# Kernel tuning notes

Hardware: AMD Instinct MI355X
Metric: run time of the kernel (lower is better)

The kernel has to match this reference:

```python
import jax, jax.numpy as jnp
import numpy as np

H = 16      # num_heads
HD = 64     # head_dim
W = 1024    # local window size
G = 256     # number of global tokens
EPS = 1e-6
NEG = -1e30


def setup_inputs() -> dict:
    key = jax.random.key(0)
    ks = jax.random.split(key, 7)
    B, S, D = 1, 8192, 1024
    inner = H * HD
    s = 0.02
    return {
        "x": jax.random.normal(ks[0], (B, S, D), jnp.float32),
        "norm_w": jnp.ones((D,), jnp.float32),
        "w_q": jax.random.normal(ks[1], (D, inner), jnp.float32) * s,
        "w_k": jax.random.normal(ks[2], (D, inner), jnp.float32) * s,
        "w_v": jax.random.normal(ks[3], (D, inner), jnp.float32) * s,
        "w_out": jax.random.normal(ks[4], (inner, D), jnp.float32) * s,
        "scorer_w": jax.random.normal(ks[5], (D, 1), jnp.float32) * s,
        "scorer_b": jnp.zeros((1,), jnp.float32),
    }


def reference(x, norm_w, w_q, w_k, w_v, w_out, scorer_w, scorer_b):
    B, S, D = x.shape
    # pre-norm (RMSNorm)
    h = x * jax.lax.rsqrt(jnp.mean(x * x, axis=-1, keepdims=True) + EPS) * norm_w

    def proj(w):  # [B,S,D] -> [B,H,S,HD]
        return jnp.einsum('bsd,de->bse', h, w).reshape(B, S, H, HD).transpose(0, 2, 1, 3)

    q, k, v = proj(w_q), proj(w_k), proj(w_v)
    scale = HD ** -0.5

    # --- local block attention (non-overlapping causal windows) ---
    nW = S // W
    qw = q.reshape(B, H, nW, W, HD)
    kw = k.reshape(B, H, nW, W, HD)
    vw = v.reshape(B, H, nW, W, HD)
    ll = jnp.einsum('bhnqd,bhnkd->bhnqk', qw, kw) * scale  # [B,H,nW,W,W]
    cm = jnp.tril(jnp.ones((W, W), bool))
    ll = jnp.where(cm, ll, NEG).reshape(B, H, S, W)

    # --- sparse global attention over top-G important tokens ---
    scores = (jnp.einsum('bsd,do->bso', h, scorer_w) + scorer_b)[..., 0]  # [B,S]
    _, idx = jax.lax.top_k(scores, G)                                     # [B,G]
    kg = jnp.take_along_axis(k, idx[:, None, :, None], axis=2)            # [B,H,G,HD]
    vg = jnp.take_along_axis(v, idx[:, None, :, None], axis=2)
    lg = jnp.einsum('bhsd,bhgd->bhsg', q, kg) * scale                     # [B,H,S,G]
    pos = jnp.arange(S)
    gmask = idx[:, None, None, :] <= pos[None, None, :, None]             # causal: global pos <= query pos
    lg = jnp.where(gmask, lg, NEG)

    # --- joint softmax over local window + global tokens ---
    attn = jax.nn.softmax(jnp.concatenate([ll, lg], axis=-1), axis=-1)    # [B,H,S,W+G]
    a_loc = attn[..., :W].reshape(B, H, nW, W, W)
    o = jnp.einsum('bhnqk,bhnkd->bhnqd', a_loc, vw).reshape(B, H, S, HD)
    o = o + jnp.einsum('bhsg,bhgd->bhsd', attn[..., W:], vg)

    o = o.transpose(0, 2, 1, 3).reshape(B, S, H * HD)
    return x + jnp.einsum('bse,ed->bsd', o, w_out)  # residual
```

## Files before the change

### kernel.cpp

```cpp
#include <hip/hip_runtime.h>
#include <stdint.h>

#define S_LEN 8192
#define DIM   1024
#define NH    16
#define HD    64
#define WIN   1024
#define GTOK  256
#define QKV_STRIDE (3 * DIM)

typedef __attribute__((ext_vector_type(8))) short bf16x8;
typedef __attribute__((ext_vector_type(4))) float f32x4;
typedef __attribute__((ext_vector_type(16))) float f32x16;
typedef unsigned short u16;

__device__ __forceinline__ u16 f2bf(float f) {
  union { float f; uint32_t u; } v; v.f = f;
  uint32_t r = v.u + 0x7fffu + ((v.u >> 16) & 1u);
  return (u16)(r >> 16);
}
__device__ __forceinline__ float bf2f(u16 b) {
  union { uint32_t u; float f; } v; v.u = ((uint32_t)b) << 16;
  return v.f;
}
__device__ __forceinline__ uint32_t cvtpk(float a, float b) {
  uint32_t r;
  asm("v_cvt_pk_bf16_f32 %0, %1, %2" : "=v"(r) : "v"(a), "v"(b));
  return r;
}

__device__ __forceinline__ void gload_lds16(const void* g, void* l) {
  __builtin_amdgcn_global_load_lds((const __attribute__((address_space(1))) void*)g,
                                   (__attribute__((address_space(3))) void*)l, 16, 0, 0);
}

__global__ __launch_bounds__(256) void rmsnorm_score_kernel(
    const float* __restrict__ x, const float* __restrict__ nw,
    const float* __restrict__ sw, const float* __restrict__ sb,
    u16* __restrict__ h, float* __restrict__ scores) {
  int row = blockIdx.x, tid = threadIdx.x;
  const float4* xr = (const float4*)(x + (size_t)row * DIM);
  float4 v = xr[tid];
  float ss = v.x * v.x + v.y * v.y + v.z * v.z + v.w * v.w;
#pragma unroll
  for (int o = 32; o >= 1; o >>= 1) ss += __shfl_xor(ss, o);
  __shared__ float red[4], red2[4];
  int wv = tid >> 6;
  if ((tid & 63) == 0) red[wv] = ss;
  __syncthreads();
  ss = red[0] + red[1] + red[2] + red[3];
  float rn = rsqrtf(ss * (1.0f / DIM) + 1e-6f);
  float4 w4 = ((const float4*)nw)[tid];
  float h0 = v.x * rn * w4.x, h1 = v.y * rn * w4.y;
  float h2 = v.z * rn * w4.z, h3 = v.w * rn * w4.w;
  uint64_t pack = (uint64_t)f2bf(h0) | ((uint64_t)f2bf(h1) << 16) |
                  ((uint64_t)f2bf(h2) << 32) | ((uint64_t)f2bf(h3) << 48);
  *(uint64_t*)(h + (size_t)row * DIM + tid * 4) = pack;
  float4 s4 = ((const float4*)sw)[tid];
  float sc = h0 * s4.x + h1 * s4.y + h2 * s4.z + h3 * s4.w;
#pragma unroll
  for (int o = 32; o >= 1; o >>= 1) sc += __shfl_xor(sc, o);
  if ((tid & 63) == 0) red2[wv] = sc;
  __syncthreads();
  if (tid == 0) scores[row] = red2[0] + red2[1] + red2[2] + red2[3] + sb[0];
}

__global__ __launch_bounds__(256) void transpose_w_kernel(
    const float* __restrict__ wq, const float* __restrict__ wk,
    const float* __restrict__ wv, const float* __restrict__ wo,
    u16* __restrict__ wqkvT, u16* __restrict__ woutT) {
  __shared__ float tile[32][33];
  int z = blockIdx.z;
  const float* src = (z == 0) ? wq : (z == 1) ? wk : (z == 2) ? wv : wo;
  u16* dst = (z < 3) ? (wqkvT + (size_t)z * DIM * DIM) : woutT;
  int tx = threadIdx.x, ty = threadIdx.y;
  int n0 = blockIdx.x * 32, k0 = blockIdx.y * 32;
#pragma unroll
  for (int i = 0; i < 4; i++)
    tile[ty + i * 8][tx] = src[(size_t)(k0 + ty + i * 8) * DIM + n0 + tx];
  __syncthreads();
#pragma unroll
  for (int i = 0; i < 4; i++)
    dst[(size_t)(n0 + ty + i * 8) * DIM + k0 + tx] = f2bf(tile[tx][ty + i * 8]);
}

__global__ __launch_bounds__(256) void topk_init_kernel(int* __restrict__ cnt) {
  cnt[blockIdx.x * 256 + threadIdx.x] = 0;
}

__global__ __launch_bounds__(256) void topk_count_kernel(
    const float* __restrict__ scores, int* __restrict__ cnt) {
  __shared__ float sj[1024];
  int jbase = blockIdx.y * 1024;
  for (int t = threadIdx.x; t < 1024; t += 256) sj[t] = scores[jbase + t];
  __syncthreads();
  int i = blockIdx.x * 256 + threadIdx.x;
  float my = scores[i];
  int c = 0;
  const float4* s4 = (const float4*)sj;
#pragma unroll 4
  for (int j = 0; j < 256; j++) {
    float4 v = s4[j];
    int b = jbase + j * 4;
    c += (v.x > my) || (v.x == my && (b + 0) < i);
    c += (v.y > my) || (v.y == my && (b + 1) < i);
    c += (v.z > my) || (v.z == my && (b + 2) < i);
    c += (v.w > my) || (v.w == my && (b + 3) < i);
  }
  if (c) atomicAdd(&cnt[i], c);
}

__global__ __launch_bounds__(256) void topk_scatter_kernel(
    const int* __restrict__ cnt, int* __restrict__ gidx) {
  int i = blockIdx.x * 256 + threadIdx.x;
  int c = cnt[i];
  if (c < GTOK) gidx[c] = i;
}

__global__ __launch_bounds__(128) void gather_kernel(
    const u16* __restrict__ qkv, const int* __restrict__ gidx,
    u16* __restrict__ kg, u16* __restrict__ vg) {
  int g = blockIdx.x, t = threadIdx.x;
  size_t src = (size_t)gidx[g] * QKV_STRIDE;
  *(bf16x8*)(kg + (size_t)g * DIM + t * 8) = *(const bf16x8*)(qkv + src + DIM + t * 8);
  *(bf16x8*)(vg + (size_t)g * DIM + t * 8) = *(const bf16x8*)(qkv + src + 2 * DIM + t * 8);
}

template <int RESID>
__global__ __launch_bounds__(256) void gemm_bt_kernel(
    const u16* __restrict__ A, const u16* __restrict__ B,
    u16* __restrict__ Cb, float* __restrict__ Cf, const float* __restrict__ X,
    int M, int N, int K) {
  __shared__ u16 aT[128 * 64];
  __shared__ u16 bT[128 * 64];
  int tid = threadIdx.x;
  int wave = tid >> 6, lane = tid & 63;
  int l15 = lane & 15, l4 = lane >> 4;
  int wr = (wave >> 1) * 64, wc = (wave & 1) * 64;
  int mbase = blockIdx.x * 128, nbase = blockIdx.y * 128;
  f32x4 acc[4][4] = {};
  for (int kt = 0; kt < K; kt += 64) {
#pragma unroll
    for (int c = 0; c < 4; c++) {
      int chunk = wave * 4 + c;
      int row = chunk * 8 + (lane >> 3);
      int col = kt + (lane & 7) * 8;
      gload_lds16(A + (size_t)(mbase + row) * K + col, aT + chunk * 512);
      gload_lds16(B + (size_t)(nbase + row) * K + col, bT + chunk * 512);
    }
    __syncthreads();
#pragma unroll
    for (int kk = 0; kk < 2; kk++) {
      bf16x8 af[4], bfr[4];
#pragma unroll
      for (int i = 0; i < 4; i++) {
        af[i]  = *(const bf16x8*)(aT + (wr + i * 16 + l15) * 64 + kk * 32 + l4 * 8);
        bfr[i] = *(const bf16x8*)(bT + (wc + i * 16 + l15) * 64 + kk * 32 + l4 * 8);
      }
#pragma unroll
      for (int i = 0; i < 4; i++)
#pragma unroll
        for (int j = 0; j < 4; j++)
          acc[i][j] = __builtin_amdgcn_mfma_f32_16x16x32_bf16(af[i], bfr[j], acc[i][j], 0, 0, 0);
    }
    __syncthreads();
  }
#pragma unroll
  for (int i = 0; i < 4; i++) {
#pragma unroll
    for (int j = 0; j < 4; j++) {
#pragma unroll
      for (int r = 0; r < 4; r++) {
        int row = mbase + wr + i * 16 + l4 * 4 + r;
        int col = nbase + wc + j * 16 + l15;
        float v = acc[i][j][r];
        if (RESID) Cf[(size_t)row * N + col] = X[(size_t)row * N + col] + v;
        else       Cb[(size_t)row * N + col] = f2bf(v);
      }
    }
  }
}

__global__ __launch_bounds__(512) void attn_kernel(
    const u16* __restrict__ qkv, const u16* __restrict__ kg,
    const u16* __restrict__ vg, const int* __restrict__ gidx,
    u16* __restrict__ o) {
  __shared__ u16 kT[2][64][72];
  __shared__ u16 vT[2][64][72];
  __shared__ int gposLds[2][64];
  const int tid = threadIdx.x, wave = tid >> 6, lane = tid & 63;
  const int l31 = lane & 31, hi = lane >> 5;
  const int win = blockIdx.x >> 1, pair = blockIdx.x & 1;
  const int wbase = win * WIN;
  const int hoff = blockIdx.y * HD;

  const int skey = tid >> 3, sd8 = (tid & 7) * 8;
  const int vcol = skey ^ ((sd8 >> 4) << 4);

  bf16x8 nk, nv;
  int ng = 0;
  {
    const u16* base = qkv + (size_t)(wbase + skey) * QKV_STRIDE + hoff + sd8;
    nk = *(const bf16x8*)(base + DIM);
    nv = *(const bf16x8*)(base + 2 * DIM);
  }

  for (int sp = 0; sp < 2; sp++) {
    const int j = sp ? (3 - pair) : pair;
    const int qsbase = wbase + j * 256;
    const int nLocal = (j + 1) * 4;
    const int nTiles = nLocal + GTOK / 64;
    const int qrow = qsbase + wave * 32 + l31;
    const int qwmax = qsbase + wave * 32 + 31;

    bf16x8 qf[4];
    {
      const float SC2 = 0.125f * 1.44269504088896f;
      const u16* qptr = qkv + (size_t)qrow * QKV_STRIDE + hoff + hi * 8;
#pragma unroll
      for (int ks = 0; ks < 4; ks++) {
        bf16x8 raw = *(const bf16x8*)(qptr + ks * 16);
        bf16x8 sc;
#pragma unroll
        for (int jj = 0; jj < 8; jj++) sc[jj] = (short)f2bf(bf2f((u16)raw[jj]) * SC2);
        qf[ks] = sc;
      }
    }

    f32x16 acc0 = {}, acc1 = {};
    float mr = -3.0e38f, lr = 0.f;

    __syncthreads();

    for (int t = 0; t < nTiles; t++) {
      const int p = t & 1;
      const bool isLocal = (t < nLocal);
      const int tbase = wbase + t * 64;
      *(bf16x8*)(&kT[p][skey][sd8]) = nk;
#pragma unroll
      for (int jj = 0; jj < 8; jj++) vT[p][sd8 + jj][vcol] = (u16)nv[jj];
      if (!isLocal && tid < 64) gposLds[p][tid] = ng;
      {
        const int nt = t + 1;
        const u16 *ksrc = nullptr, *vsrc = nullptr;
        if (nt < nLocal) {
          const u16* base = qkv + (size_t)(wbase + nt * 64 + skey) * QKV_STRIDE + hoff + sd8;
          ksrc = base + DIM; vsrc = base + 2 * DIM;
        } else if (nt < nTiles) {
          size_t grow = (size_t)((nt - nLocal) * 64 + skey) * DIM + hoff + sd8;
          ksrc = kg + grow; vsrc = vg + grow;
          if (tid < 64) ng = gidx[(nt - nLocal) * 64 + tid];
        } else if (sp == 0) {
          const u16* base = qkv + (size_t)(wbase + skey) * QKV_STRIDE + hoff + sd8;
          ksrc = base + DIM; vsrc = base + 2 * DIM;
        }
        if (ksrc) { nk = *(const bf16x8*)(ksrc); nv = *(const bf16x8*)(vsrc); }
      }
      __syncthreads();

      if (isLocal && tbase > qwmax) continue;

      float sv[32];
      __builtin_amdgcn_s_setprio(1);
#pragma unroll
      for (int kb = 0; kb < 2; kb++) {
        const u16* krow = &kT[p][kb * 32 + l31][hi * 8];
        bf16x8 k0 = *(const bf16x8*)(krow);
        bf16x8 k1 = *(const bf16x8*)(krow + 16);
        bf16x8 k2 = *(const bf16x8*)(krow + 32);
        bf16x8 k3 = *(const bf16x8*)(krow + 48);
        f32x16 z = {};
        z = __builtin_amdgcn_mfma_f32_32x32x16_bf16(k0, qf[0], z, 0, 0, 0);
        z = __builtin_amdgcn_mfma_f32_32x32x16_bf16(k1, qf[1], z, 0, 0, 0);
        z = __builtin_amdgcn_mfma_f32_32x32x16_bf16(k2, qf[2], z, 0, 0, 0);
        z = __builtin_amdgcn_mfma_f32_32x32x16_bf16(k3, qf[3], z, 0, 0, 0);
#pragma unroll
        for (int r = 0; r < 16; r++) sv[kb * 16 + r] = z[r];
      }
      __builtin_amdgcn_s_setprio(0);

      if (isLocal) {
        const int lim = qrow - tbase;
        if (lim < 63) {
#pragma unroll
          for (int kb = 0; kb < 2; kb++)
#pragma unroll
            for (int r = 0; r < 16; r++) {
              int crow = kb * 32 + (r & 3) + 8 * (r >> 2) + 4 * hi;
              if (crow > lim) sv[kb * 16 + r] = -3.0e38f;
            }
        }
      } else {
#pragma unroll
        for (int kb = 0; kb < 2; kb++)
#pragma unroll
          for (int r = 0; r < 16; r++) {
            int kpos = gposLds[p][kb * 32 + (r & 3) + 8 * (r >> 2) + 4 * hi];
            if (kpos > qrow) sv[kb * 16 + r] = -3.0e38f;
          }
      }

      float m0 = sv[0], m1 = sv[1], m2 = sv[2], m3 = sv[3];
#pragma unroll
      for (int i = 4; i < 32; i += 4) {
        m0 = fmaxf(m0, sv[i]);     m1 = fmaxf(m1, sv[i + 1]);
        m2 = fmaxf(m2, sv[i + 2]); m3 = fmaxf(m3, sv[i + 3]);
      }
      float vmax = fmaxf(fmaxf(m0, m1), fmaxf(m2, m3));
      vmax = fmaxf(vmax, __shfl_xor(vmax, 32));
      if (__any(vmax > mr + 11.0f)) {
        float mn = fmaxf(mr, vmax);
        float al = exp2f(mr - mn);
        lr *= al;
        mr = mn;
#pragma unroll
        for (int i = 0; i < 16; i++) { acc0[i] *= al; acc1[i] *= al; }
      }
      float s0 = 0.f, s1 = 0.f, s2 = 0.f, s3 = 0.f;
#pragma unroll
      for (int i = 0; i < 32; i += 4) {
        float p0 = exp2f(sv[i] - mr),     p1 = exp2f(sv[i + 1] - mr);
        float p2 = exp2f(sv[i + 2] - mr), p3 = exp2f(sv[i + 3] - mr);
        sv[i] = p0; sv[i + 1] = p1; sv[i + 2] = p2; sv[i + 3] = p3;
        s0 += p0; s1 += p1; s2 += p2; s3 += p3;
      }
      float ps = (s0 + s1) + (s2 + s3);
      ps += __shfl_xor(ps, 32);
      lr += ps;

      bf16x8 pf[4];
#pragma unroll
      for (int q4 = 0; q4 < 4; q4++) {
        int b = q4 * 8;
        uint32_t w0 = cvtpk(sv[b + 0], sv[b + 1]);
        uint32_t w1 = cvtpk(sv[b + 2], sv[b + 3]);
        uint32_t w2 = cvtpk(sv[b + 4], sv[b + 5]);
        uint32_t w3 = cvtpk(sv[b + 6], sv[b + 7]);
        uint32_t w0s = __shfl_xor((int)w0, 32), w2s = __shfl_xor((int)w2, 32);
        uint32_t w1s = __shfl_xor((int)w1, 32), w3s = __shfl_xor((int)w3, 32);
        union { uint32_t w[4]; bf16x8 v; } u;
        u.w[0] = hi ? w2s : w0;
        u.w[1] = hi ? w3s : w1;
        u.w[2] = hi ? w2 : w0s;
        u.w[3] = hi ? w3 : w1s;
        pf[q4] = u.v;
      }

      __builtin_amdgcn_s_setprio(1);
#pragma unroll
      for (int dblk = 0; dblk < 2; dblk++) {
        const int swz = (dblk * 2 + (l31 >> 4)) << 4;
        const u16* vrow = &vT[p][dblk * 32 + l31][0];
        f32x16 a = dblk ? acc1 : acc0;
#pragma unroll
        for (int ksg = 0; ksg < 4; ksg++) {
          bf16x8 vf = *(const bf16x8*)(vrow + ((ksg * 16 + hi * 8) ^ swz));
          a = __builtin_amdgcn_mfma_f32_32x32x16_bf16(vf, pf[ksg], a, 0, 0, 0);
        }
        if (dblk) acc1 = a; else acc0 = a;
      }
      __builtin_amdgcn_s_setprio(0);
    }

    float inv = 1.0f / lr;
#pragma unroll
    for (int dblk = 0; dblk < 2; dblk++) {
      f32x16 a = dblk ? acc1 : acc0;
#pragma unroll
      for (int g = 0; g < 4; g++) {
        uint64_t pk = (uint64_t)f2bf(a[g * 4 + 0] * inv)
                    | ((uint64_t)f2bf(a[g * 4 + 1] * inv) << 16)
                    | ((uint64_t)f2bf(a[g * 4 + 2] * inv) << 32)
                    | ((uint64_t)f2bf(a[g * 4 + 3] * inv) << 48);
        *(uint64_t*)(o + (size_t)qrow * DIM + hoff + dblk * 32 + g * 8 + 4 * hi) = pk;
      }
    }
  }
}

extern "C" void kernel_launch(void* const* d_in, const int* in_sizes, int n_in,
                              void* d_out, int out_size, void* d_ws, size_t ws_size,
                              hipStream_t stream) {
  const float* x  = (const float*)d_in[0];
  const float* nw = (const float*)d_in[1];
  const float* wq = (const float*)d_in[2];
  const float* wk = (const float*)d_in[3];
  const float* wv = (const float*)d_in[4];
  const float* wo = (const float*)d_in[5];
  const float* sw = (const float*)d_in[6];
  const float* sb = (const float*)d_in[7];
  float* out = (float*)d_out;

  char* ws = (char*)d_ws;
  size_t off = 0;
  auto alloc = [&](size_t b) {
    char* p = ws + off;
    off = (off + b + 255) & ~(size_t)255;
    return p;
  };
  u16*   h      = (u16*)alloc((size_t)S_LEN * DIM * 2);
  u16*   wqkvT  = (u16*)alloc((size_t)3 * DIM * DIM * 2);
  u16*   woutT  = (u16*)alloc((size_t)DIM * DIM * 2);
  u16*   qkv    = (u16*)alloc((size_t)S_LEN * 3 * DIM * 2);
  u16*   obuf   = (u16*)alloc((size_t)S_LEN * DIM * 2);
  float* scores = (float*)alloc((size_t)S_LEN * 4);
  int*   gidx   = (int*)alloc((size_t)GTOK * 4);
  int*   cnt    = (int*)alloc((size_t)S_LEN * 4);
  u16*   kgbuf  = (u16*)alloc((size_t)GTOK * DIM * 2);
  u16*   vgbuf  = (u16*)alloc((size_t)GTOK * DIM * 2);

  transpose_w_kernel<<<dim3(32, 32, 4), dim3(32, 8), 0, stream>>>(wq, wk, wv, wo, wqkvT, woutT);
  rmsnorm_score_kernel<<<dim3(S_LEN), dim3(256), 0, stream>>>(x, nw, sw, sb, h, scores);
  topk_init_kernel<<<dim3(S_LEN / 256), dim3(256), 0, stream>>>(cnt);
  topk_count_kernel<<<dim3(32, 8), dim3(256), 0, stream>>>(scores, cnt);
  topk_scatter_kernel<<<dim3(S_LEN / 256), dim3(256), 0, stream>>>(cnt, gidx);
  gemm_bt_kernel<0><<<dim3(64, 24), dim3(256), 0, stream>>>(h, wqkvT, qkv, nullptr, nullptr,
                                                            S_LEN, 3 * DIM, DIM);
  gather_kernel<<<dim3(GTOK), dim3(128), 0, stream>>>(qkv, gidx, kgbuf, vgbuf);
  attn_kernel<<<dim3(16, NH), dim3(512), 0, stream>>>(qkv, kgbuf, vgbuf, gidx, obuf);
  gemm_bt_kernel<1><<<dim3(64, 8), dim3(256), 0, stream>>>(obuf, woutT, nullptr, out, x,
                                                           S_LEN, DIM, DIM);
}
```

Measured before the change: 230.2 us.

## Replace GEMM with 256x256-tile double-buffered swizzled LDS kernel

Swaps the 128x128 single-buffered GEMM for a 512-thread kernel that computes 256x256 output tiles. It prefetches the next K-slice into a second LDS buffer while the MFMAs run on the current one, and XOR-swizzles LDS chunks to avoid bank conflicts. It also raises wave priority around the MFMA bursts. The goals are more data reuse per byte loaded and hiding global-load latency. The costs are 128KB of LDS per block, which allows only one block per CU, and far fewer blocks: the output projection launches only 128, which can leave many CUs idle.

Result: no change. 230.3 us (+0.0%).

```diff
diff --git a/kernel.cpp b/kernel.cpp
--- a/kernel.cpp
+++ b/kernel.cpp
@@ -127,53 +127,96 @@
 }
 
 template <int RESID>
-__global__ __launch_bounds__(256) void gemm_bt_kernel(
+__global__ __launch_bounds__(512, 2) void gemm256_kernel(
     const u16* __restrict__ A, const u16* __restrict__ B,
     u16* __restrict__ Cb, float* __restrict__ Cf, const float* __restrict__ X,
     int M, int N, int K) {
-  __shared__ u16 aT[128 * 64];
-  __shared__ u16 bT[128 * 64];
-  int tid = threadIdx.x;
-  int wave = tid >> 6, lane = tid & 63;
-  int l15 = lane & 15, l4 = lane >> 4;
-  int wr = (wave >> 1) * 64, wc = (wave & 1) * 64;
-  int mbase = blockIdx.x * 128, nbase = blockIdx.y * 128;
-  f32x4 acc[4][4] = {};
-  for (int kt = 0; kt < K; kt += 64) {
-#pragma unroll
-    for (int c = 0; c < 4; c++) {
-      int chunk = wave * 4 + c;
-      int row = chunk * 8 + (lane >> 3);
-      int col = kt + (lane & 7) * 8;
-      gload_lds16(A + (size_t)(mbase + row) * K + col, aT + chunk * 512);
-      gload_lds16(B + (size_t)(nbase + row) * K + col, bT + chunk * 512);
-    }
+  __shared__ u16 As[2][256 * 64];
+  __shared__ u16 Bs[2][256 * 64];
+  const int tid = threadIdx.x;
+  const int wave = tid >> 6, lane = tid & 63;
+  const int l15 = lane & 15, l4 = lane >> 4;
+  const int wr = wave >> 2, wc = wave & 3;
+  const int mbase = blockIdx.x * 256, nbase = blockIdx.y * 256;
+
+  const int srow = (lane >> 3);
+  const int schunk = lane & 7;
+  const int gchunk8 = (schunk ^ srow) * 8;
+
+  f32x4 acc[8][4] = {};
+
+  const int nt = K >> 6;
+#pragma unroll
+  for (int l = 0; l < 4; l++) {
+    int rbase = (wave * 4 + l) * 8;
+    int row = rbase + srow;
+    gload_lds16(A + (size_t)(mbase + row) * K + gchunk8,
+                &As[0][(size_t)(wave * 4 + l) * 512]);
+    gload_lds16(B + (size_t)(nbase + row) * K + gchunk8,
+                &Bs[0][(size_t)(wave * 4 + l) * 512]);
+  }
+  asm volatile("s_waitcnt vmcnt(0)" ::: "memory");
+  __syncthreads();
+
+  for (int t = 0; t < nt; t++) {
+    const int p = t & 1;
+    if (t + 1 < nt) {
+      const int kt = (t + 1) << 6;
+#pragma unroll
+      for (int l = 0; l < 4; l++) {
+        int rbase = (wave * 4 + l) * 8;
+        int row = rbase + srow;
+        gload_lds16(A + (size_t)(mbase + row) * K + kt + gchunk8,
+                    &As[p ^ 1][(size_t)(wave * 4 + l) * 512]);
+        gload_lds16(B + (size_t)(nbase + row) * K + kt + gchunk8,
+                    &Bs[p ^ 1][(size_t)(wave * 4 + l) * 512]);
+      }
+    }
+    const u16* Ab = &As[p][0];
+    const u16* Bb = &Bs[p][0];
+    bf16x8 bfr[4][2];
+#pragma unroll
+    for (int nf = 0; nf < 4; nf++) {
+      int row = wc * 64 + nf * 16 + l15;
+#pragma unroll
+      for (int kk = 0; kk < 2; kk++)
+        bfr[nf][kk] = *(const bf16x8*)(Bb + row * 64 + (((kk * 4 + l4) ^ (l15 & 7)) * 8));
+    }
+#pragma unroll
+    for (int mh = 0; mh < 2; mh++) {
+      bf16x8 af[4][2];
+#pragma unroll
+      for (int mi = 0; mi < 4; mi++) {
+        int row = wr * 128 + (mh * 4 + mi) * 16 + l15;
+#pragma unroll
+        for (int kk = 0; kk < 2; kk++)
+          af[mi][kk] = *(const bf16x8*)(Ab + row * 64 + (((kk * 4 + l4) ^ (l15 & 7)) * 8));
+      }
+      __builtin_amdgcn_s_setprio(1);
+#pragma unroll
+      for (int mi = 0; mi < 4; mi++)
+#pragma unroll
+        for (int nf = 0; nf < 4; nf++)
+#pragma unroll
+          for (int kk = 0; kk < 2; kk++)
+            acc[mh * 4 + mi][nf] =
+                __builtin_amdgcn_mfma_f32_16x16x32_bf16(af[mi][kk], bfr[nf][kk],
+                                                        acc[mh * 4 + mi][nf], 0, 0, 0);
+      __builtin_amdgcn_s_setprio(0);
+    }
+    asm volatile("s_waitcnt vmcnt(0)" ::: "memory");
     __syncthreads();
-#pragma unroll
-    for (int kk = 0; kk < 2; kk++) {
-      bf16x8 af[4], bfr[4];
-#pragma unroll
-      for (int i = 0; i < 4; i++) {
-        af[i]  = *(const bf16x8*)(aT + (wr + i * 16 + l15) * 64 + kk * 32 + l4 * 8);
-        bfr[i] = *(const bf16x8*)(bT + (wc + i * 16 + l15) * 64 + kk * 32 + l4 * 8);
-      }
-#pragma unroll
-      for (int i = 0; i < 4; i++)
-#pragma unroll
-        for (int j = 0; j < 4; j++)
-          acc[i][j] = __builtin_amdgcn_mfma_f32_16x16x32_bf16(af[i], bfr[j], acc[i][j], 0, 0, 0);
-    }
-    __syncthreads();
-  }
-#pragma unroll
-  for (int i = 0; i < 4; i++) {
-#pragma unroll
-    for (int j = 0; j < 4; j++) {
+  }
+
+#pragma unroll
+  for (int mf = 0; mf < 8; mf++) {
+#pragma unroll
+    for (int nf = 0; nf < 4; nf++) {
 #pragma unroll
       for (int r = 0; r < 4; r++) {
-        int row = mbase + wr + i * 16 + l4 * 4 + r;
-        int col = nbase + wc + j * 16 + l15;
-        float v = acc[i][j][r];
+        int row = mbase + wr * 128 + mf * 16 + l4 * 4 + r;
+        int col = nbase + wc * 64 + nf * 16 + l15;
+        float v = acc[mf][nf][r];
         if (RESID) Cf[(size_t)row * N + col] = X[(size_t)row * N + col] + v;
         else       Cb[(size_t)row * N + col] = f2bf(v);
       }
@@ -414,10 +457,10 @@
   topk_init_kernel<<<dim3(S_LEN / 256), dim3(256), 0, stream>>>(cnt);
   topk_count_kernel<<<dim3(32, 8), dim3(256), 0, stream>>>(scores, cnt);
   topk_scatter_kernel<<<dim3(S_LEN / 256), dim3(256), 0, stream>>>(cnt, gidx);
-  gemm_bt_kernel<0><<<dim3(64, 24), dim3(256), 0, stream>>>(h, wqkvT, qkv, nullptr, nullptr,
+  gemm256_kernel<0><<<dim3(32, 12), dim3(512), 0, stream>>>(h, wqkvT, qkv, nullptr, nullptr,
                                                             S_LEN, 3 * DIM, DIM);
   gather_kernel<<<dim3(GTOK), dim3(128), 0, stream>>>(qkv, gidx, kgbuf, vgbuf);
   attn_kernel<<<dim3(16, NH), dim3(512), 0, stream>>>(qkv, kgbuf, vgbuf, gidx, obuf);
-  gemm_bt_kernel<1><<<dim3(64, 8), dim3(256), 0, stream>>>(obuf, woutT, nullptr, out, x,
+  gemm256_kernel<1><<<dim3(32, 4), dim3(512), 0, stream>>>(obuf, woutT, nullptr, out, x,
                                                            S_LEN, DIM, DIM);
 }
```
